# Kernel optimization log

Measured on AMD Instinct MI355X. Metric: run time of the kernel, lower is better.

The kernel has to match this reference:

```python
import jax, jax.numpy as jnp
import numpy as np

N = 100000      # nodes
E = 3200000     # edges (avg degree 32)
DIN, DH, DOUT = 256, 256, 64
K = 10          # propagation hops


def _uniform(key, shape, fan_in):
    b = 1.0 / np.sqrt(fan_in)
    return jax.random.uniform(key, shape, jnp.float32, -b, b)


def setup_inputs() -> dict:
    key = jax.random.key(0)
    ks = jax.random.split(key, 8)
    x = jax.random.normal(ks[0], (N, DIN), jnp.float32)
    edge_index = jax.random.randint(ks[1], (2, E), 0, N, dtype=jnp.int64)
    W1 = _uniform(ks[2], (DIN, DH), DIN)
    b1 = _uniform(ks[3], (DH,), DIN)
    W2 = _uniform(ks[4], (DH, DOUT), DH)
    b2 = _uniform(ks[5], (DOUT,), DH)
    proj_w = _uniform(ks[6], (DOUT,), DOUT)
    proj_b = _uniform(ks[7], (), DOUT)
    return {"x": x, "edge_index": edge_index, "W1": W1, "b1": b1,
            "W2": W2, "b2": b2, "proj_w": proj_w, "proj_b": proj_b}


def _gcn_norm(edge_index, num_nodes):
    # add self-loops with weight 1, symmetric normalization deg^-1/2 A deg^-1/2
    loops = jnp.arange(num_nodes, dtype=edge_index.dtype)
    row = jnp.concatenate([edge_index[0], loops])
    col = jnp.concatenate([edge_index[1], loops])
    w = jnp.ones(row.shape[0], jnp.float32)
    deg = jax.ops.segment_sum(w, col, num_segments=num_nodes)
    dinv = jnp.where(deg > 0, jax.lax.rsqrt(deg), 0.0)
    norm = dinv[row] * dinv[col]  # edge weight is 1
    return row, col, norm


def reference(x, edge_index, W1, b1, W2, b2, proj_w, proj_b):
    h = jax.nn.relu(x @ W1 + b1)
    h = h @ W2 + b2                               # [N, DOUT]
    row, col, norm = _gcn_norm(edge_index, N)
    preds = [h]
    for _ in range(K):
        h = jax.ops.segment_sum(norm[:, None] * h[row], col, num_segments=N)
        preds.append(h)
    pps = jnp.stack(preds, axis=1)                # [N, K+1, DOUT]
    score = jax.nn.sigmoid(pps @ proj_w + proj_b) # [N, K+1]
    out = jnp.einsum('nk,nkc->nc', score, pps)    # adaptive hop pooling
    return out
```

## Files before the change

### kernel.cpp

```cpp
#include <hip/hip_runtime.h>
#include <hip/hip_bf16.h>
#include <math.h>


#define WAVE 64
#define NBLK 1024
#define RS 520

__device__ inline float bf2f(unsigned short u) {
    union { unsigned int i; float f; } v; v.i = ((unsigned int)u) << 16; return v.f;
}
__device__ inline unsigned short f2bf(float f) {
    __hip_bfloat16 b = __float2bfloat16(f);
    union { __hip_bfloat16 b; unsigned short u; } v; v.b = b; return v.u;
}

typedef __attribute__((ext_vector_type(8))) short bf16x8;
typedef __attribute__((ext_vector_type(16))) float f32x16;

__global__ void detect_kernel(const unsigned* __restrict__ e, int* __restrict__ sflag) {
    __shared__ int any;
    if (threadIdx.x == 0) any = 0;
    __syncthreads();
    unsigned nz = 0;
    int t = threadIdx.x;
    for (int i = 0; i < 8; ++i) nz |= e[(size_t)(t * 8 + i) * 2 + 1];
    if (nz) atomicOr(&any, 1);
    __syncthreads();
    if (t == 0) *sflag = any ? 1 : 2;
}

__global__ void passA_kernel(const int* __restrict__ eidx, const int* __restrict__ sflag,
                             int* __restrict__ blk_cnt, int E, int NB, int EPB) {
    __shared__ int lh[512];
    int t = threadIdx.x, blk = blockIdx.x;
    for (int i = t; i < NB; i += 256) lh[i] = 0;
    __syncthreads();
    int s = *sflag;
    int base = blk * EPB;
    int end = base + EPB; if (end > E) end = E;
    for (int e = base + t; e < end; e += 256) {
        int c = eidx[(size_t)s * (size_t)(E + e)];
        atomicAdd(&lh[c >> 8], 1);
    }
    __syncthreads();
    for (int i = t; i < NB; i += 256)
        blk_cnt[(size_t)blk * NB + i] = lh[i];
}

__global__ void scan1_kernel(const int* __restrict__ in, int* __restrict__ out,
                             int* __restrict__ bsums, int n) {
    __shared__ int s[256];
    int t = threadIdx.x;
    int idx = blockIdx.x * 1024 + t * 4;
    int x0 = (idx + 0 < n) ? in[idx + 0] : 0;
    int x1 = (idx + 1 < n) ? in[idx + 1] : 0;
    int x2 = (idx + 2 < n) ? in[idx + 2] : 0;
    int x3 = (idx + 3 < n) ? in[idx + 3] : 0;
    int lsum = x0 + x1 + x2 + x3;
    s[t] = lsum;
    __syncthreads();
    for (int o = 1; o < 256; o <<= 1) {
        int v = (t >= o) ? s[t - o] : 0;
        __syncthreads();
        if (t >= o) s[t] += v;
        __syncthreads();
    }
    int excl = s[t] - lsum;
    if (idx + 0 < n) out[idx + 0] = excl;
    if (idx + 1 < n) out[idx + 1] = excl + x0;
    if (idx + 2 < n) out[idx + 2] = excl + x0 + x1;
    if (idx + 3 < n) out[idx + 3] = excl + x0 + x1 + x2;
    if (t == 255) bsums[blockIdx.x] = s[255];
}

__global__ void scan2g_kernel(int* __restrict__ bsums, int nb) {
    __shared__ int part[256];
    int t = threadIdx.x;
    int v[4]; int run = 0;
    #pragma unroll
    for (int j = 0; j < 4; ++j) {
        int i = t * 4 + j;
        int x = (i < nb) ? bsums[i] : 0;
        v[j] = run; run += x;
    }
    part[t] = run;
    __syncthreads();
    for (int o = 1; o < 256; o <<= 1) {
        int x = (t >= o) ? part[t - o] : 0;
        __syncthreads();
        if (t >= o) part[t] += x;
        __syncthreads();
    }
    int excl = part[t] - run;
    #pragma unroll
    for (int j = 0; j < 4; ++j) {
        int i = t * 4 + j;
        if (i < nb) bsums[i] = excl + v[j];
    }
}

__global__ void scan3_kernel(int* __restrict__ arr, const int* __restrict__ bsums,
                             int n, int total) {
    int t = threadIdx.x;
    int idx = blockIdx.x * 1024 + t * 4;
    int add = bsums[blockIdx.x];
    #pragma unroll
    for (int i = 0; i < 4; ++i)
        if (idx + i < n) arr[idx + i] += add;
    if (blockIdx.x == 0 && t == 0) arr[n] = total;
}

__global__ void passB_kernel(const int* __restrict__ eidx, const int* __restrict__ sflag,
                             const int* __restrict__ pbase, int2* __restrict__ pairs,
                             int E, int NB, int EPB) {
    __shared__ int lcur[512];
    int t = threadIdx.x, blk = blockIdx.x;
    for (int i = t; i < NB; i += 256) lcur[i] = pbase[(size_t)blk * NB + i];
    __syncthreads();
    int s = *sflag;
    int base = blk * EPB;
    int end = base + EPB; if (end > E) end = E;
    for (int e = base + t; e < end; e += 256) {
        int r = eidx[(size_t)s * (size_t)e];
        int c = eidx[(size_t)s * (size_t)(E + e)];
        int pos = atomicAdd(&lcur[c >> 8], 1);
        pairs[pos] = make_int2(r, c);
    }
}

__global__ void passD_kernel(const int2* __restrict__ pairs, const int* __restrict__ pbase,
                             int* __restrict__ cnt, int N, int NB) {
    __shared__ int lcnt[256];
    int b = blockIdx.x, t = threadIdx.x;
    lcnt[t] = 0;
    __syncthreads();
    for (int blk = t; blk < NBLK; blk += 256) {
        int w0 = pbase[(size_t)blk * NB + b];
        int w1 = pbase[(size_t)blk * NB + b + 1];
        for (int i = w0; i < w1; ++i)
            atomicAdd(&lcnt[pairs[i].y & 255], 1);
    }
    __syncthreads();
    int node = b * 256 + t;
    if (node < N) cnt[node] = lcnt[t];
}

__global__ void dinv_kernel(const int* __restrict__ cnt, float* __restrict__ dinv, int n) {
    int i = blockIdx.x * blockDim.x + threadIdx.x;
    if (i < n) dinv[i] = rsqrtf((float)(cnt[i] + 1));
}

__global__ void passC_kernel(const int2* __restrict__ pairs, const int* __restrict__ pbase,
                             const int* __restrict__ offs, int* __restrict__ csr_src,
                             int N, int NB) {
    __shared__ int lcur[256];
    int b = blockIdx.x, t = threadIdx.x;
    int node = b * 256 + t;
    lcur[t] = (node < N) ? offs[node] : 0;
    __syncthreads();
    for (int blk = t; blk < NBLK; blk += 256) {
        int w0 = pbase[(size_t)blk * NB + b];
        int w1 = pbase[(size_t)blk * NB + b + 1];
        for (int i = w0; i < w1; ++i) {
            int2 p = pairs[i];
            int pos = atomicAdd(&lcur[p.y & 255], 1);
            csr_src[pos] = p.x;
        }
    }
}

__global__ void wconv_kernel(const float* __restrict__ W, unsigned short* __restrict__ Wf,
                             int K, int Nn) {
    int i = blockIdx.x * blockDim.x + threadIdx.x;
    if (i >= K * Nn) return;
    int k = i / Nn, n = i - k * Nn;
    Wf[(size_t)(k >> 3) * Nn * 8 + n * 8 + (k & 7)] = f2bf(W[i]);
}

__global__ __launch_bounds__(256, 4) void mlp_fused(
        const float* __restrict__ x,
        const unsigned short* __restrict__ W1f,
        const float* __restrict__ b1,
        const unsigned short* __restrict__ W2f,
        const float* __restrict__ b2,
        const float* __restrict__ dinv,
        const float* __restrict__ pw, const float* __restrict__ pb,
        float* __restrict__ out, unsigned short* __restrict__ g,
        int M) {
    __shared__ unsigned short xfrag[4 * RS];
    __shared__ unsigned short h1frag[32 * RS];
    __shared__ float pools[2][2][2][16];

    int tid = threadIdx.x;
    int wave = tid >> 6, lane = tid & 63;
    int half = lane >> 5, l31 = lane & 31;
    int rt = wave & 1;
    int cw = wave >> 1;
    int bm = blockIdx.x * 64;

    f32x16 acc1[4] = {};

    float4 xv[2];
    #pragma unroll
    for (int i = 0; i < 2; ++i) {
        int f = i * 256 + tid;
        int row = f >> 3, c4 = (f & 7) * 4;
        int grow = bm + row;
        xv[i] = (grow < M) ? *(const float4*)(x + (size_t)grow * 256 + c4)
                           : make_float4(0.f, 0.f, 0.f, 0.f);
    }

    for (int it = 0; it < 8; ++it) {
        #pragma unroll
        for (int i = 0; i < 2; ++i) {
            int f = i * 256 + tid;
            int row = f >> 3, c4 = (f & 7) * 4;
            int region = c4 >> 3, off = c4 & 7;
            ushort4 u;
            u.x = f2bf(xv[i].x); u.y = f2bf(xv[i].y);
            u.z = f2bf(xv[i].z); u.w = f2bf(xv[i].w);
            *(ushort4*)&xfrag[region * RS + row * 8 + off] = u;
        }
        __syncthreads();
        if (it < 7) {
            int k0 = (it + 1) * 32;
            #pragma unroll
            for (int i = 0; i < 2; ++i) {
                int f = i * 256 + tid;
                int row = f >> 3, c4 = (f & 7) * 4;
                int grow = bm + row;
                xv[i] = (grow < M) ? *(const float4*)(x + (size_t)grow * 256 + k0 + c4)
                                   : make_float4(0.f, 0.f, 0.f, 0.f);
            }
        }
        #pragma unroll
        for (int s = 0; s < 2; ++s) {
            int region = it * 4 + s * 2 + half;
            bf16x8 a = *(bf16x8*)&xfrag[(s * 2 + half) * RS + (rt * 32 + l31) * 8];
            #pragma unroll
            for (int j = 0; j < 4; ++j) {
                int ch = cw * 128 + j * 32 + l31;
                bf16x8 b = *(const bf16x8*)(W1f + (size_t)region * 2048 + ch * 8);
                acc1[j] = __builtin_amdgcn_mfma_f32_32x32x16_bf16(a, b, acc1[j], 0, 0, 0);
            }
        }
        __syncthreads();
    }

    #pragma unroll
    for (int j = 0; j < 4; ++j) {
        int ch = cw * 128 + j * 32 + l31;
        float bb = b1[ch];
        int region = ch >> 3, off = ch & 7;
        #pragma unroll
        for (int reg = 0; reg < 16; ++reg) {
            int rowin = (reg & 3) + 8 * (reg >> 2) + 4 * half;
            int row = rt * 32 + rowin;
            float v = fmaxf(acc1[j][reg] + bb, 0.f);
            h1frag[region * RS + row * 8 + off] = f2bf(v);
        }
    }
    __syncthreads();

    int rt2 = wave >> 1, ct2 = wave & 1;
    f32x16 acc2 = {};
    #pragma unroll
    for (int s = 0; s < 16; ++s) {
        bf16x8 a = *(bf16x8*)&h1frag[(s * 2 + half) * RS + (rt2 * 32 + l31) * 8];
        bf16x8 b = *(const bf16x8*)(W2f + (size_t)(s * 2 + half) * 512 + (ct2 * 32 + l31) * 8);
        acc2 = __builtin_amdgcn_mfma_f32_32x32x16_bf16(a, b, acc2, 0, 0, 0);
    }

    float bb = b2[ct2 * 32 + l31];
    float pwv = pw[ct2 * 32 + l31];
    float pbv = pb[0];
    float hreg[16];
    #pragma unroll
    for (int reg = 0; reg < 16; ++reg) {
        float h = acc2[reg] + bb;
        hreg[reg] = h;
        float d = h * pwv;
        d += __shfl_xor(d, 1, 64);
        d += __shfl_xor(d, 2, 64);
        d += __shfl_xor(d, 4, 64);
        d += __shfl_xor(d, 8, 64);
        d += __shfl_xor(d, 16, 64);
        if (l31 == 0) pools[rt2][ct2][half][reg] = d;
    }
    __syncthreads();
    #pragma unroll
    for (int reg = 0; reg < 16; ++reg) {
        int rowin = (reg & 3) + 8 * (reg >> 2) + 4 * half;
        int row = bm + rt2 * 32 + rowin;
        float d = pools[rt2][0][half][reg] + pools[rt2][1][half][reg];
        float sg = 1.f / (1.f + __expf(-(d + pbv)));
        float h = hreg[reg];
        if (row < M) {
            float dv = dinv[row];
            out[(size_t)row * 64 + ct2 * 32 + l31] = sg * h;
            g[(size_t)row * 64 + ct2 * 32 + l31]   = f2bf(dv * h);
        }
    }
}

__global__ void spmm_kernel(const int* __restrict__ offs, const int* __restrict__ src,
                            const float* __restrict__ dinv,
                            const __hip_bfloat16* __restrict__ gin,
                            __hip_bfloat16* __restrict__ gout,
                            float* __restrict__ out,
                            const float* __restrict__ pw, const float* __restrict__ pb,
                            int n) {
    int wid = (blockIdx.x * blockDim.x + threadIdx.x) >> 6;
    int lane = threadIdx.x & 63;
    if (wid >= n) return;
    int c = __builtin_amdgcn_readfirstlane(wid);
    int e = __builtin_amdgcn_readfirstlane(offs[c]);
    int eend = __builtin_amdgcn_readfirstlane(offs[c + 1]);
    float acc = 0.f;
    while (e < eend && (e & 3)) {
        acc += __bfloat162float(gin[(size_t)src[e] * 64 + lane]);
        ++e;
    }
    for (; e + 7 < eend; e += 8) {
        int4 sa = *(const int4*)(src + e);
        int4 sb = *(const int4*)(src + e + 4);
        float v0 = __bfloat162float(gin[(size_t)sa.x * 64 + lane]);
        float v1 = __bfloat162float(gin[(size_t)sa.y * 64 + lane]);
        float v2 = __bfloat162float(gin[(size_t)sa.z * 64 + lane]);
        float v3 = __bfloat162float(gin[(size_t)sa.w * 64 + lane]);
        float v4 = __bfloat162float(gin[(size_t)sb.x * 64 + lane]);
        float v5 = __bfloat162float(gin[(size_t)sb.y * 64 + lane]);
        float v6 = __bfloat162float(gin[(size_t)sb.z * 64 + lane]);
        float v7 = __bfloat162float(gin[(size_t)sb.w * 64 + lane]);
        acc += ((v0 + v1) + (v2 + v3)) + ((v4 + v5) + (v6 + v7));
    }
    for (; e + 3 < eend; e += 4) {
        int4 sa = *(const int4*)(src + e);
        float v0 = __bfloat162float(gin[(size_t)sa.x * 64 + lane]);
        float v1 = __bfloat162float(gin[(size_t)sa.y * 64 + lane]);
        float v2 = __bfloat162float(gin[(size_t)sa.z * 64 + lane]);
        float v3 = __bfloat162float(gin[(size_t)sa.w * 64 + lane]);
        acc += (v0 + v1) + (v2 + v3);
    }
    for (; e < eend; ++e) acc += __bfloat162float(gin[(size_t)src[e] * 64 + lane]);

    float dc = dinv[c];
    float h = dc * (acc + __bfloat162float(gin[(size_t)c * 64 + lane]));
    gout[(size_t)c * 64 + lane] = __float2bfloat16(dc * h);
    float d = h * pw[lane];
    #pragma unroll
    for (int o = 32; o > 0; o >>= 1) d += __shfl_xor(d, o, 64);
    float sg = 1.f / (1.f + __expf(-(d + pb[0])));
    out[(size_t)c * 64 + lane] += sg * h;
}

extern "C" void kernel_launch(void* const* d_in, const int* in_sizes, int n_in,
                              void* d_out, int out_size, void* d_ws, size_t ws_size,
                              hipStream_t stream) {
    const float* x  = (const float*)d_in[0];
    const int* eidx = (const int*)d_in[1];
    const float* W1 = (const float*)d_in[2];
    const float* b1 = (const float*)d_in[3];
    const float* W2 = (const float*)d_in[4];
    const float* b2 = (const float*)d_in[5];
    const float* pw = (const float*)d_in[6];
    const float* pb = (const float*)d_in[7];
    float* out = (float*)d_out;

    const int N = in_sizes[0] / 256;
    const int E = in_sizes[1] / 2;
    const int NB = (N + 255) >> 8;
    const int EPB = (E + NBLK - 1) / NBLK;
    const int M = NB * NBLK;

    size_t woff = 0;
    auto alloc = [&](size_t bytes) -> void* {
        void* p = (char*)d_ws + woff;
        woff += (bytes + 255) & ~(size_t)255;
        return p;
    };
    int*   sflag   = (int*)alloc(4);
    int*   cnt     = (int*)alloc((size_t)N * 4);
    float* dinv    = (float*)alloc((size_t)N * 4);
    int*   offs    = (int*)alloc(((size_t)N + 1) * 4);
    int*   bsums   = (int*)alloc(1024 * 4);
    int*   bsums2  = (int*)alloc(1024 * 4);
    int*   pbase   = (int*)alloc(((size_t)M + 1) * 4);
    int*   csr_src = (int*)alloc((size_t)E * 4);
    int2*  pairs   = (int2*)alloc((size_t)E * 8);
    unsigned short* W1f = (unsigned short*)alloc((size_t)256 * 256 * 2);
    unsigned short* W2f = (unsigned short*)alloc((size_t)64 * 256 * 2);
    __hip_bfloat16* gA = (__hip_bfloat16*)alloc((size_t)N * 64 * 2);
    __hip_bfloat16* gB = (__hip_bfloat16*)alloc((size_t)N * 64 * 2);

    detect_kernel<<<1, 256, 0, stream>>>((const unsigned*)eidx, sflag);

    passA_kernel<<<NBLK, 256, 0, stream>>>(eidx, sflag, pbase, E, NB, EPB);
    int nb2 = (M + 1023) / 1024;
    scan1_kernel<<<nb2, 256, 0, stream>>>(pbase, pbase, bsums2, M);
    scan2g_kernel<<<1, 256, 0, stream>>>(bsums2, nb2);
    scan3_kernel<<<nb2, 256, 0, stream>>>(pbase, bsums2, M, E);
    passB_kernel<<<NBLK, 256, 0, stream>>>(eidx, sflag, pbase, pairs, E, NB, EPB);
    passD_kernel<<<NB, 256, 0, stream>>>(pairs, pbase, cnt, N, NB);
    dinv_kernel<<<(N + 255) / 256, 256, 0, stream>>>(cnt, dinv, N);
    int nb1 = (N + 1023) / 1024;
    scan1_kernel<<<nb1, 256, 0, stream>>>(cnt, offs, bsums, N);
    scan2g_kernel<<<1, 256, 0, stream>>>(bsums, nb1);
    scan3_kernel<<<nb1, 256, 0, stream>>>(offs, bsums, N, E);
    passC_kernel<<<NB, 256, 0, stream>>>(pairs, pbase, offs, csr_src, N, NB);

    wconv_kernel<<<(256 * 256 + 255) / 256, 256, 0, stream>>>(W1, W1f, 256, 256);
    wconv_kernel<<<(64 * 256 + 255) / 256, 256, 0, stream>>>(W2, W2f, 256, 64);
    int gb = (N + 63) / 64;
    mlp_fused<<<gb, 256, 0, stream>>>(x, W1f, b1, W2f, b2, dinv, pw, pb,
                                      out, (unsigned short*)gA, N);

    int nwb = (N + 3) / 4;
    __hip_bfloat16* gin = gA;
    __hip_bfloat16* gout = gB;
    for (int k = 0; k < 10; ++k) {
        spmm_kernel<<<nwb, 256, 0, stream>>>(offs, csr_src, dinv, gin, gout, out, pw, pb, N);
        __hip_bfloat16* t = gin; gin = gout; gout = t;
    }
}
```

Measured before the change: 1.097 ms.

## Process four edges per wave with 8-byte gathers in SpMM hop kernel

Restructures the per-node SpMM gather so each wave splits into four 16-lane groups. Each group handles a different edge and loads 4 bf16 features per lane as one 8-byte access, instead of one 2-byte load per lane per edge. Partial sums are combined with cross-group shuffles, and the output and next-hop stores are vectorized. This raises memory-level parallelism and the bytes per gather instruction for the hop propagation. In exchange it adds masked padding work for low-degree tails, several shuffles, and leaves only a quarter of lanes active during the stores.

```diff
diff --git a/kernel.cpp b/kernel.cpp
--- a/kernel.cpp
+++ b/kernel.cpp
@@ -13,6 +13,12 @@
 __device__ inline unsigned short f2bf(float f) {
     __hip_bfloat16 b = __float2bfloat16(f);
     union { __hip_bfloat16 b; unsigned short u; } v; v.b = b; return v.u;
+}
+__device__ inline float bflo(unsigned u) {
+    union { unsigned i; float f; } v; v.i = u << 16; return v.f;
+}
+__device__ inline float bfhi(unsigned u) {
+    union { unsigned i; float f; } v; v.i = u & 0xffff0000u; return v.f;
 }
 
 typedef __attribute__((ext_vector_type(8))) short bf16x8;
@@ -306,53 +312,65 @@
 
 __global__ void spmm_kernel(const int* __restrict__ offs, const int* __restrict__ src,
                             const float* __restrict__ dinv,
-                            const __hip_bfloat16* __restrict__ gin,
-                            __hip_bfloat16* __restrict__ gout,
+                            const unsigned* __restrict__ gin,
+                            unsigned short* __restrict__ gout,
                             float* __restrict__ out,
                             const float* __restrict__ pw, const float* __restrict__ pb,
                             int n) {
     int wid = (blockIdx.x * blockDim.x + threadIdx.x) >> 6;
     int lane = threadIdx.x & 63;
     if (wid >= n) return;
+    int g = lane >> 4;
+    int q = lane & 15;
     int c = __builtin_amdgcn_readfirstlane(wid);
-    int e = __builtin_amdgcn_readfirstlane(offs[c]);
+    int e0   = __builtin_amdgcn_readfirstlane(offs[c]);
     int eend = __builtin_amdgcn_readfirstlane(offs[c + 1]);
-    float acc = 0.f;
-    while (e < eend && (e & 3)) {
-        acc += __bfloat162float(gin[(size_t)src[e] * 64 + lane]);
-        ++e;
-    }
-    for (; e + 7 < eend; e += 8) {
-        int4 sa = *(const int4*)(src + e);
-        int4 sb = *(const int4*)(src + e + 4);
-        float v0 = __bfloat162float(gin[(size_t)sa.x * 64 + lane]);
-        float v1 = __bfloat162float(gin[(size_t)sa.y * 64 + lane]);
-        float v2 = __bfloat162float(gin[(size_t)sa.z * 64 + lane]);
-        float v3 = __bfloat162float(gin[(size_t)sa.w * 64 + lane]);
-        float v4 = __bfloat162float(gin[(size_t)sb.x * 64 + lane]);
-        float v5 = __bfloat162float(gin[(size_t)sb.y * 64 + lane]);
-        float v6 = __bfloat162float(gin[(size_t)sb.z * 64 + lane]);
-        float v7 = __bfloat162float(gin[(size_t)sb.w * 64 + lane]);
-        acc += ((v0 + v1) + (v2 + v3)) + ((v4 + v5) + (v6 + v7));
-    }
-    for (; e + 3 < eend; e += 4) {
-        int4 sa = *(const int4*)(src + e);
-        float v0 = __bfloat162float(gin[(size_t)sa.x * 64 + lane]);
-        float v1 = __bfloat162float(gin[(size_t)sa.y * 64 + lane]);
-        float v2 = __bfloat162float(gin[(size_t)sa.z * 64 + lane]);
-        float v3 = __bfloat162float(gin[(size_t)sa.w * 64 + lane]);
-        acc += (v0 + v1) + (v2 + v3);
-    }
-    for (; e < eend; ++e) acc += __bfloat162float(gin[(size_t)src[e] * 64 + lane]);
+
+    float a0 = 0.f, a1 = 0.f, a2 = 0.f, a3 = 0.f;
+    for (int e = e0; e < eend; e += 32) {
+        #pragma unroll
+        for (int i = 0; i < 8; ++i) {
+            int ei = e + i * 4 + g;
+            int ec = (ei < eend) ? ei : (eend - 1);
+            float m = (ei < eend) ? 1.f : 0.f;
+            int s = src[ec];
+            uint2 v = *(const uint2*)(gin + (size_t)s * 32 + q * 2);
+            a0 = fmaf(m, bflo(v.x), a0);
+            a1 = fmaf(m, bfhi(v.x), a1);
+            a2 = fmaf(m, bflo(v.y), a2);
+            a3 = fmaf(m, bfhi(v.y), a3);
+        }
+    }
+
+    a0 += __shfl_xor(a0, 16, 64); a0 += __shfl_xor(a0, 32, 64);
+    a1 += __shfl_xor(a1, 16, 64); a1 += __shfl_xor(a1, 32, 64);
+    a2 += __shfl_xor(a2, 16, 64); a2 += __shfl_xor(a2, 32, 64);
+    a3 += __shfl_xor(a3, 16, 64); a3 += __shfl_xor(a3, 32, 64);
+
+    uint2 sv = *(const uint2*)(gin + (size_t)c * 32 + q * 2);
+    a0 += bflo(sv.x); a1 += bfhi(sv.x);
+    a2 += bflo(sv.y); a3 += bfhi(sv.y);
 
     float dc = dinv[c];
-    float h = dc * (acc + __bfloat162float(gin[(size_t)c * 64 + lane]));
-    gout[(size_t)c * 64 + lane] = __float2bfloat16(dc * h);
-    float d = h * pw[lane];
-    #pragma unroll
-    for (int o = 32; o > 0; o >>= 1) d += __shfl_xor(d, o, 64);
+    float h0 = dc * a0, h1 = dc * a1, h2 = dc * a2, h3 = dc * a3;
+
+    float4 pv = *(const float4*)(pw + q * 4);
+    float d = h0 * pv.x + h1 * pv.y + h2 * pv.z + h3 * pv.w;
+    d += __shfl_xor(d, 1, 64);
+    d += __shfl_xor(d, 2, 64);
+    d += __shfl_xor(d, 4, 64);
+    d += __shfl_xor(d, 8, 64);
     float sg = 1.f / (1.f + __expf(-(d + pb[0])));
-    out[(size_t)c * 64 + lane] += sg * h;
+
+    if (g == 0) {
+        ushort4 gw;
+        gw.x = f2bf(dc * h0); gw.y = f2bf(dc * h1);
+        gw.z = f2bf(dc * h2); gw.w = f2bf(dc * h3);
+        *(ushort4*)(gout + (size_t)c * 64 + q * 4) = gw;
+        float4 o = *(float4*)(out + (size_t)c * 64 + q * 4);
+        o.x += sg * h0; o.y += sg * h1; o.z += sg * h2; o.w += sg * h3;
+        *(float4*)(out + (size_t)c * 64 + q * 4) = o;
+    }
 }
 
 extern "C" void kernel_launch(void* const* d_in, const int* in_sizes, int n_in,
@@ -391,8 +409,8 @@
     int2*  pairs   = (int2*)alloc((size_t)E * 8);
     unsigned short* W1f = (unsigned short*)alloc((size_t)256 * 256 * 2);
     unsigned short* W2f = (unsigned short*)alloc((size_t)64 * 256 * 2);
-    __hip_bfloat16* gA = (__hip_bfloat16*)alloc((size_t)N * 64 * 2);
-    __hip_bfloat16* gB = (__hip_bfloat16*)alloc((size_t)N * 64 * 2);
+    unsigned short* gA = (unsigned short*)alloc((size_t)N * 64 * 2);
+    unsigned short* gB = (unsigned short*)alloc((size_t)N * 64 * 2);
 
     detect_kernel<<<1, 256, 0, stream>>>((const unsigned*)eidx, sflag);
 
@@ -414,13 +432,14 @@
     wconv_kernel<<<(64 * 256 + 255) / 256, 256, 0, stream>>>(W2, W2f, 256, 64);
     int gb = (N + 63) / 64;
     mlp_fused<<<gb, 256, 0, stream>>>(x, W1f, b1, W2f, b2, dinv, pw, pb,
-                                      out, (unsigned short*)gA, N);
+                                      out, gA, N);
 
     int nwb = (N + 3) / 4;
-    __hip_bfloat16* gin = gA;
-    __hip_bfloat16* gout = gB;
+    unsigned short* gin = gA;
+    unsigned short* gout = gB;
     for (int k = 0; k < 10; ++k) {
-        spmm_kernel<<<nwb, 256, 0, stream>>>(offs, csr_src, dinv, gin, gout, out, pw, pb, N);
-        __hip_bfloat16* t = gin; gin = gout; gout = t;
-    }
-}
+        spmm_kernel<<<nwb, 256, 0, stream>>>(offs, csr_src, dinv,
+                                             (const unsigned*)gin, gout, out, pw, pb, N);
+        unsigned short* t = gin; gin = gout; gout = t;
+    }
+}
```

Measured after the change: 980.3 us. -10.6%, faster.
